# Performance work log

Hardware: AMD Instinct MI355X
Metric: run time of the kernel (lower is better)

The kernel has to match this reference:

```python
import jax, jax.numpy as jnp
import numpy as np

B, T, C = 2, 4096, 768
H = 12
D = C // H  # head_dim = 64
SCALE = np.sqrt(D).astype(np.float32)


def setup_inputs() -> dict:
    key = jax.random.key(0)
    ks = jax.random.split(key, 5)
    s = 0.02
    return {
        "x": jax.random.normal(ks[0], (B, T, C), dtype=jnp.float32),
        "Wqkv": jax.random.normal(ks[1], (C, 3 * C), dtype=jnp.float32) * s,
        "bqkv": jnp.zeros((3 * C,), dtype=jnp.float32),
        "Wout": jax.random.normal(ks[2], (C, C), dtype=jnp.float32) * s,
        "bout": jnp.zeros((C,), dtype=jnp.float32),
    }


def reference(x, Wqkv, bqkv, Wout, bout):
    Bx, Tx, Cx = x.shape
    qkv = x @ Wqkv + bqkv                                   # [B,T,3C]
    qkv = qkv.reshape(Bx, Tx, 3, H, D)
    q, k, v = [jnp.moveaxis(qkv[:, :, i], 2, 1) for i in range(3)]  # each [B,H,T,D]
    attn = jnp.einsum("bhqd,bhkd->bhqk", q, k) / SCALE      # [B,H,T,T]
    causal = jnp.tril(jnp.ones((Tx, Tx), dtype=bool))
    attn = jnp.where(causal, attn, jnp.float32(-jnp.inf))
    attn = jax.nn.softmax(attn, axis=-1)
    out = jnp.einsum("bhqk,bhkd->bhqd", attn, v)            # [B,H,T,D]
    out = jnp.moveaxis(out, 1, 2).reshape(Bx, Tx, Cx)       # [B,T,C]
    return out @ Wout + bout
```

## Files before the change

### kernel.cpp

```cpp
#include <hip/hip_runtime.h>
#include <hip/hip_bf16.h>

#define T_DIM 4096
#define H_N 12
#define D_H 64
#define C_DIM 768
#define B_N 2

typedef short bf16x8 __attribute__((ext_vector_type(8)));
typedef float f32x4 __attribute__((ext_vector_type(4)));
typedef float f32x16 __attribute__((ext_vector_type(16)));

__device__ __forceinline__ short f2bf(float f) {
    union { float f; unsigned u; } x; x.f = f;
    unsigned r = x.u + 0x7fffu + ((x.u >> 16) & 1u);
    return (short)(r >> 16);
}
__device__ __forceinline__ unsigned pk2bf(float a, float b) {
    union { float f; unsigned u; } x, y; x.f = a; y.f = b;
    unsigned ua = x.u + 0x7fffu + ((x.u >> 16) & 1u);
    unsigned ub = y.u + 0x7fffu + ((y.u >> 16) & 1u);
    return (ua >> 16) | (ub & 0xffff0000u);
}
__device__ __forceinline__ unsigned pktrunc(float lo, float hi) {
    union { float f; unsigned u; } a, b; a.f = lo; b.f = hi;
    return __builtin_amdgcn_perm(b.u, a.u, 0x07060302u);
}
__device__ __forceinline__ float bf2f(short s) {
    union { unsigned u; float f; } x; x.u = ((unsigned)(unsigned short)s) << 16;
    return x.f;
}

__device__ __forceinline__ void async_copy16(const void* g, void* l) {
    __builtin_amdgcn_global_load_lds(
        (const __attribute__((address_space(1))) unsigned*)g,
        (__attribute__((address_space(3))) unsigned*)l, 16, 0, 0);
}

#define Q_SCALE 0.18033688011112042f

#define CHUNK 1152
#define UNITS_PB 74
#define SLOTS_PB 74

__device__ __forceinline__ void wtrans_body(
    const float* __restrict__ W, short* __restrict__ Wt, int K, int N,
    int bx, int by, int tid)
{
    const int wave = tid >> 6, lane = tid & 63;
    const int n = bx * 256 + wave * 64 + lane;
    const int k0 = by * 128;
    for (int k = k0; k < k0 + 128; k += 8) {
        unsigned pk[4];
#pragma unroll
        for (int j = 0; j < 4; ++j)
            pk[j] = pk2bf(W[(size_t)(k + 2 * j) * N + n],
                          W[(size_t)(k + 2 * j + 1) * N + n]);
        *(uint4*)(Wt + (size_t)n * K + k) = *(uint4*)pk;
    }
}

__global__ __launch_bounds__(256) void prep_kernel(
    const float* __restrict__ x, short* __restrict__ xb,
    const float* __restrict__ Wqkv, short* __restrict__ Wqkvb,
    const float* __restrict__ Wout, short* __restrict__ Woutb)
{
    const int bid = blockIdx.x;
    const int tid = threadIdx.x;
    if (bid < 3072) {
        size_t i = ((size_t)bid * 256 + tid) * 8;
        float4 a = *(const float4*)(x + i);
        float4 b = *(const float4*)(x + i + 4);
        unsigned pk[4];
        pk[0] = pk2bf(a.x, a.y); pk[1] = pk2bf(a.z, a.w);
        pk[2] = pk2bf(b.x, b.y); pk[3] = pk2bf(b.z, b.w);
        *(uint4*)(xb + i) = *(uint4*)pk;
    } else if (bid < 3126) {
        int u = bid - 3072;
        wtrans_body(Wqkv, Wqkvb, 768, 2304, u % 9, u / 9, tid);
    } else {
        int u = bid - 3126;
        wtrans_body(Wout, Woutb, 768, 768, u % 3, u / 3, tid);
    }
}

__global__ __launch_bounds__(256) void qkv_kernel(
    const short* __restrict__ xb, const short* __restrict__ Wb,
    const float* __restrict__ bias,
    short* __restrict__ Qo, short* __restrict__ Ko, short* __restrict__ Vto)
{
    __shared__ short As[128 * 32];
    __shared__ short Bs[128 * 32];
    __shared__ short Vs[64][136];

    const int tid  = threadIdx.x;
    const int wave = tid >> 6, lane = tid & 63;
    const int quad = lane >> 4, l16 = lane & 15;
    const int wm = wave >> 1, wn = wave & 1;
    const int lin = blockIdx.x;
    const int xcd = lin & 7, idx = lin >> 3;
    const int m0 = (xcd * 8 + (idx & 7)) * 128;
    const int n0 = (idx >> 3) * 128;
    const int lrow = lane >> 2, lcc = lane & 3;

    f32x4 acc[4][4];
#pragma unroll
    for (int i = 0; i < 4; ++i)
#pragma unroll
        for (int j = 0; j < 4; ++j) acc[i][j] = (f32x4){0.f, 0.f, 0.f, 0.f};

    for (int k0 = 0; k0 < 768; k0 += 32) {
        __syncthreads();
#pragma unroll
        for (int i = 0; i < 2; ++i) {
            const int sbase = wave * 128 + i * 64;
            const int row = wave * 32 + i * 16 + lrow;
            async_copy16(xb + (size_t)(m0 + row) * 768 + k0 + lcc * 8, &As[sbase * 8]);
            async_copy16(Wb + (size_t)(n0 + row) * 768 + k0 + lcc * 8, &Bs[sbase * 8]);
        }
        asm volatile("s_waitcnt vmcnt(0)" ::: "memory");
        __syncthreads();

        bf16x8 af[4], bfr[4];
#pragma unroll
        for (int t = 0; t < 4; ++t)
            af[t] = *(const bf16x8*)&As[(wm * 64 + t * 16 + l16) * 32 + quad * 8];
#pragma unroll
        for (int t = 0; t < 4; ++t)
            bfr[t] = *(const bf16x8*)&Bs[(wn * 64 + t * 16 + l16) * 32 + quad * 8];
#pragma unroll
        for (int mt = 0; mt < 4; ++mt)
#pragma unroll
            for (int nt = 0; nt < 4; ++nt)
                acc[mt][nt] = __builtin_amdgcn_mfma_f32_16x16x32_bf16(
                    af[mt], bfr[nt], acc[mt][nt], 0, 0, 0);
    }

    if (n0 < 1536) {
#pragma unroll
        for (int nt = 0; nt < 4; ++nt) {
            int n = n0 + wn * 64 + nt * 16 + l16;
            float bv = bias[n];
            int which = n >= 768;
            int cw = n - which * 768;
            int h = cw >> 6, d = cw & 63;
            float scale = which ? 1.0f : Q_SCALE;
            short* dst = which ? Ko : Qo;
#pragma unroll
            for (int mt = 0; mt < 4; ++mt) {
#pragma unroll
                for (int reg = 0; reg < 4; ++reg) {
                    int m = m0 + wm * 64 + mt * 16 + quad * 4 + reg;
                    int b = m >> 12, t = m & 4095;
                    dst[(size_t)((b * H_N + h) * T_DIM + t) * D_H + d] =
                        f2bf((acc[mt][nt][reg] + bv) * scale);
                }
            }
        }
    } else {
        const int b = m0 >> 12, t0 = m0 & 4095;
        for (int p = 0; p < 2; ++p) {
            if (wn == p) {
#pragma unroll
                for (int nt = 0; nt < 4; ++nt) {
                    int n = n0 + wn * 64 + nt * 16 + l16;
                    float bv = bias[n];
#pragma unroll
                    for (int mt = 0; mt < 4; ++mt)
#pragma unroll
                        for (int reg = 0; reg < 4; ++reg)
                            Vs[nt * 16 + l16][wm * 64 + mt * 16 + quad * 4 + reg] =
                                f2bf(acc[mt][nt][reg] + bv);
                }
            }
            __syncthreads();
            int hh = ((n0 - 1536) >> 6) + p;
#pragma unroll
            for (int cc = tid; cc < 512; cc += 256) {
                int d = cc >> 3, part = cc & 7;
                bf16x8 v0 = *(const bf16x8*)&Vs[d][part * 16];
                bf16x8 v1 = *(const bf16x8*)&Vs[d][part * 16 + 8];
                size_t dst = ((size_t)(b * H_N + hh) * D_H + d) * T_DIM + t0 + part * 16;
                *(bf16x8*)(Vto + dst) = v0;
                *(bf16x8*)(Vto + dst + 8) = v1;
            }
            __syncthreads();
        }
    }
}

template<bool EDGE>
__device__ __forceinline__ void attn_tile(
    const short* __restrict__ Kb, const short* __restrict__ Vb,
    const bf16x8 (&qf)[4], const bf16x8& ones,
    f32x16& oacc0, f32x16& oacc1, f32x16& lacc,
    int kv0, int row0, int l32, int hi, int qrow)
{
#pragma unroll
    for (int sub = 0; sub < 2; ++sub) {
        if (EDGE && (kv0 + sub * 32 > row0 + 31)) continue;

        f32x16 sacc;
#pragma unroll
        for (int r = 0; r < 16; ++r) sacc[r] = 0.f;
        const int R = sub * 32 + l32;
        __builtin_amdgcn_s_setprio(1);
#pragma unroll
        for (int dk = 0; dk < 4; ++dk) {
            bf16x8 kf = *(const bf16x8*)
                &Kb[(R * 8 + ((dk * 2 + hi) ^ (R & 7))) * 8];
            sacc = __builtin_amdgcn_mfma_f32_32x32x16_bf16(kf, qf[dk], sacc, 0, 0, 0);
        }
        __builtin_amdgcn_s_setprio(0);

        if (EDGE && (kv0 + sub * 32 + 31 > row0)) {
#pragma unroll
            for (int r = 0; r < 16; ++r) {
                int kvg = kv0 + sub * 32 + (r & 3) + 8 * (r >> 2) + 4 * hi;
                if (kvg > qrow) sacc[r] = -1e30f;
            }
        }

        unsigned w[8];
#pragma unroll
        for (int r2 = 0; r2 < 8; ++r2)
            w[r2] = pktrunc(exp2f(sacc[2 * r2]), exp2f(sacc[2 * r2 + 1]));

        asm volatile("v_permlane32_swap_b32 %0, %1" : "+v"(w[0]), "+v"(w[2]));
        asm volatile("v_permlane32_swap_b32 %0, %1" : "+v"(w[1]), "+v"(w[3]));
        asm volatile("v_permlane32_swap_b32 %0, %1" : "+v"(w[4]), "+v"(w[6]));
        asm volatile("v_permlane32_swap_b32 %0, %1" : "+v"(w[5]), "+v"(w[7]));
        union { unsigned u[4]; bf16x8 v; } af0, af1;
        af0.u[0] = w[0]; af0.u[1] = w[1]; af0.u[2] = w[2]; af0.u[3] = w[3];
        af1.u[0] = w[4]; af1.u[1] = w[5]; af1.u[2] = w[6]; af1.u[3] = w[7];

        __builtin_amdgcn_s_setprio(1);
        lacc = __builtin_amdgcn_mfma_f32_32x32x16_bf16(af0.v, ones, lacc, 0, 0, 0);
        lacc = __builtin_amdgcn_mfma_f32_32x32x16_bf16(af1.v, ones, lacc, 0, 0, 0);

#pragma unroll
        for (int kh = 0; kh < 2; ++kh) {
            bf16x8 pa = kh ? af1.v : af0.v;
#pragma unroll
            for (int dt = 0; dt < 2; ++dt) {
                int Rv = dt * 32 + l32;
                bf16x8 vf = *(const bf16x8*)
                    &Vb[(Rv * 8 + ((sub * 4 + kh * 2 + hi) ^ (Rv & 7))) * 8];
                f32x16& oa = dt ? oacc1 : oacc0;
                oa = __builtin_amdgcn_mfma_f32_32x32x16_bf16(pa, vf, oa, 0, 0, 0);
            }
        }
        __builtin_amdgcn_s_setprio(0);
    }
}

__global__ __launch_bounds__(256, 4) void attn_partial_kernel(
    const short* __restrict__ Q, const short* __restrict__ K,
    const short* __restrict__ Vt, short* __restrict__ Opart,
    float* __restrict__ Lbuf)
{
    __shared__ short KsT[2][4096];
    __shared__ short VsT[2][4096];

    const int tid  = threadIdx.x;
    const int wave = tid >> 6, lane = tid & 63;
    const int l32 = lane & 31, hi = lane >> 5;
    const int lin = blockIdx.x;
    const int xcd = lin & 7, idx = lin >> 3;
    const int bh = xcd + ((idx / UNITS_PB) << 3);
    const int rr = idx % UNITS_PB;

    int qj, ci;
    if (rr < 9)       { qj = 9 + rr; ci = 0; }
    else if (rr < 27) { int u = rr - 9;  qj = 18 + (u >> 1); ci = u & 1; }
    else if (rr < 42) { int u = rr - 27; qj = 27 + u / 3; ci = u % 3; }
    else if (rr < 54) { int t = rr - 42; int m = 8 - t / 3; int idxm = t % 3;
                        qj = m + 9 * idxm; ci = idxm; }
    else              { int t = rr - 54; int m = 4 - (t >> 2); int idxm = t & 3;
                        qj = m + 9 * idxm; ci = idxm; }

    const int q0 = qj * 128;
    const int kvStart = ci * CHUNK;
    const int kvEnd = min(kvStart + CHUNK, q0 + 128);
    const int ntiles = (kvEnd - kvStart) >> 6;
    const int off = (qj < 9)  ? qj
                  : (qj < 18) ? 9 + (qj - 9) * 2
                  : (qj < 27) ? 27 + (qj - 18) * 3
                              : 54 + (qj - 27) * 4;
    const int s = bh * SLOTS_PB + off + ci;
    const size_t base = (size_t)bh * T_DIM * D_H;
    const int row0 = q0 + wave * 32;
    const int qrow = row0 + l32;

    const int nfull = min(ntiles, max(0, (row0 - kvStart + 1) >> 6));

    bf16x8 qf[4];
#pragma unroll
    for (int dk = 0; dk < 4; ++dk)
        qf[dk] = *(const bf16x8*)(
            Q + base + (size_t)(row0 + l32) * 64 + dk * 16 + hi * 8);

    bf16x8 ones;
#pragma unroll
    for (int j = 0; j < 8; ++j) ones[j] = (short)0x3F80;

    f32x16 oacc0, oacc1, lacc;
#pragma unroll
    for (int r = 0; r < 16; ++r) { oacc0[r] = 0.f; oacc1[r] = 0.f; lacc[r] = 0.f; }

    const int srow = (wave * 128 + lane) >> 3;
    const int scol0 = (lane & 7) ^ (srow & 7);
    const int srow1 = (wave * 128 + 64 + lane) >> 3;
    const int scol1 = (lane & 7) ^ (srow1 & 7);

    {
        const int kv0 = kvStart;
        async_copy16(K + base + (size_t)(kv0 + srow) * 64 + scol0 * 8,
                     &KsT[0][(wave * 128) * 8]);
        async_copy16(Vt + base + (size_t)srow * T_DIM + kv0 + scol0 * 8,
                     &VsT[0][(wave * 128) * 8]);
        async_copy16(K + base + (size_t)(kv0 + srow1) * 64 + scol1 * 8,
                     &KsT[0][(wave * 128 + 64) * 8]);
        async_copy16(Vt + base + (size_t)srow1 * T_DIM + kv0 + scol1 * 8,
                     &VsT[0][(wave * 128 + 64) * 8]);
    }

    int buf = 0;
    for (int it = 0; it < ntiles; ++it) {
        const int kv0 = kvStart + it * 64;

        asm volatile("s_waitcnt vmcnt(0)" ::: "memory");
        asm volatile("s_barrier" ::: "memory");

        if (it + 1 < ntiles) {
            const int kn = kv0 + 64;
            async_copy16(K + base + (size_t)(kn + srow) * 64 + scol0 * 8,
                         &KsT[buf ^ 1][(wave * 128) * 8]);
            async_copy16(Vt + base + (size_t)srow * T_DIM + kn + scol0 * 8,
                         &VsT[buf ^ 1][(wave * 128) * 8]);
            async_copy16(K + base + (size_t)(kn + srow1) * 64 + scol1 * 8,
                         &KsT[buf ^ 1][(wave * 128 + 64) * 8]);
            async_copy16(Vt + base + (size_t)srow1 * T_DIM + kn + scol1 * 8,
                         &VsT[buf ^ 1][(wave * 128 + 64) * 8]);
        }

        if (it < nfull) {
            attn_tile<false>(&KsT[buf][0], &VsT[buf][0], qf, ones,
                             oacc0, oacc1, lacc, kv0, row0, l32, hi, qrow);
        } else if (kv0 <= row0 + 31) {
            attn_tile<true>(&KsT[buf][0], &VsT[buf][0], qf, ones,
                            oacc0, oacc1, lacc, kv0, row0, l32, hi, qrow);
        }
        buf ^= 1;
    }

    short* op = Opart + (size_t)s * 8192;
#pragma unroll
    for (int r = 0; r < 16; ++r) {
        int qr = wave * 32 + (r & 3) + 8 * (r >> 2) + 4 * hi;
        op[qr * 64 + l32]      = f2bf(oacc0[r]);
        op[qr * 64 + 32 + l32] = f2bf(oacc1[r]);
    }
    if (l32 == 0) {
#pragma unroll
        for (int r = 0; r < 16; ++r)
            Lbuf[s * 128 + wave * 32 + (r & 3) + 8 * (r >> 2) + 4 * hi] = lacc[r];
    }
}

__global__ __launch_bounds__(256) void combine_kernel(
    const short* __restrict__ Opart, const float* __restrict__ Lbuf,
    short* __restrict__ O)
{
    const int tid = threadIdx.x;
    const int qi = blockIdx.x, bh = blockIdx.y;
    const int b = bh / H_N, h = bh - b * H_N;
    const int r = tid >> 2, cg = (tid & 3) * 16;
    const int qj = qi >> 1;
    const int riu = (qi & 1) * 64 + r;
    const int off = (qj < 9)  ? qj
                  : (qj < 18) ? 9 + (qj - 9) * 2
                  : (qj < 27) ? 27 + (qj - 18) * 3
                              : 54 + (qj - 27) * 4;
    const int nc = qj / 9 + 1;
    const int s0 = bh * SLOTS_PB + off;

    float l = 0.f;
    float res[16];
#pragma unroll
    for (int j = 0; j < 16; ++j) res[j] = 0.f;

    for (int ci = 0; ci < nc; ++ci) {
        const int su = s0 + ci;
        l += Lbuf[su * 128 + riu];
        const short* p = Opart + (size_t)su * 8192 + riu * 64 + cg;
        bf16x8 a0 = *(const bf16x8*)p;
        bf16x8 a1 = *(const bf16x8*)(p + 8);
#pragma unroll
        for (int j = 0; j < 8; ++j) { res[j] += bf2f(a0[j]); res[8 + j] += bf2f(a1[j]); }
    }

    float inv = 1.0f / l;
    unsigned pk[8];
#pragma unroll
    for (int j = 0; j < 8; ++j) pk[j] = pk2bf(res[2 * j] * inv, res[2 * j + 1] * inv);
    size_t o = ((size_t)b * T_DIM + qi * 64 + r) * C_DIM + h * 64 + cg;
    *(uint4*)(O + o)     = *(uint4*)&pk[0];
    *(uint4*)(O + o + 8) = *(uint4*)&pk[4];
}

__global__ __launch_bounds__(256) void out_kernel(
    const short* __restrict__ A, const short* __restrict__ Wb,
    const float* __restrict__ bias, float* __restrict__ out)
{
    __shared__ short As[64 * 32];
    __shared__ short Bs[128 * 32];

    const int tid  = threadIdx.x;
    const int wave = tid >> 6, lane = tid & 63;
    const int quad = lane >> 4, l16 = lane & 15;
    const int wm = wave >> 1, wn = wave & 1;
    const int lin = blockIdx.x;
    const int xcd = lin & 7, idx = lin >> 3;
    const int m0 = (xcd * 16 + (idx & 15)) * 64;
    const int n0 = (idx >> 4) * 128;
    const int lrow = lane >> 2, lcc = lane & 3;
    const int aRow = wave * 16 + lrow;

    f32x4 acc[2][4];
#pragma unroll
    for (int i = 0; i < 2; ++i)
#pragma unroll
        for (int j = 0; j < 4; ++j) acc[i][j] = (f32x4){0.f, 0.f, 0.f, 0.f};

    for (int k0 = 0; k0 < 768; k0 += 32) {
        __syncthreads();
        async_copy16(A + (size_t)(m0 + aRow) * 768 + k0 + lcc * 8, &As[wave * 512]);
#pragma unroll
        for (int i = 0; i < 2; ++i) {
            const int sbase = wave * 128 + i * 64;
            const int row = wave * 32 + i * 16 + lrow;
            async_copy16(Wb + (size_t)(n0 + row) * 768 + k0 + lcc * 8, &Bs[sbase * 8]);
        }
        asm volatile("s_waitcnt vmcnt(0)" ::: "memory");
        __syncthreads();

        bf16x8 af[2], bfr[4];
#pragma unroll
        for (int t = 0; t < 2; ++t)
            af[t] = *(const bf16x8*)&As[(wm * 32 + t * 16 + l16) * 32 + quad * 8];
#pragma unroll
        for (int t = 0; t < 4; ++t)
            bfr[t] = *(const bf16x8*)&Bs[(wn * 64 + t * 16 + l16) * 32 + quad * 8];
#pragma unroll
        for (int mt = 0; mt < 2; ++mt)
#pragma unroll
            for (int nt = 0; nt < 4; ++nt)
                acc[mt][nt] = __builtin_amdgcn_mfma_f32_16x16x32_bf16(
                    af[mt], bfr[nt], acc[mt][nt], 0, 0, 0);
    }

#pragma unroll
    for (int nt = 0; nt < 4; ++nt) {
        int n = n0 + wn * 64 + nt * 16 + l16;
        float bv = bias[n];
#pragma unroll
        for (int mt = 0; mt < 2; ++mt) {
#pragma unroll
            for (int reg = 0; reg < 4; ++reg) {
                int m = m0 + wm * 32 + mt * 16 + quad * 4 + reg;
                out[(size_t)m * 768 + n] = acc[mt][nt][reg] + bv;
            }
        }
    }
}

extern "C" void kernel_launch(void* const* d_in, const int* in_sizes, int n_in,
                              void* d_out, int out_size, void* d_ws, size_t ws_size,
                              hipStream_t stream) {
    const float* x    = (const float*)d_in[0];
    const float* Wqkv = (const float*)d_in[1];
    const float* bqkv = (const float*)d_in[2];
    const float* Wout = (const float*)d_in[3];
    const float* bout = (const float*)d_in[4];
    float* out = (float*)d_out;

    const size_t per = (size_t)B_N * H_N * T_DIM * D_H;
    short* Q      = (short*)d_ws;
    short* K      = Q + per;
    short* Vt     = K + per;
    short* Woutb  = Vt + per;
    short* xb     = Woutb + (size_t)768 * 768;
    short* Wqkvb  = xb + per;
    short* Opart  = xb;
    float* Lbuf   = (float*)(Opart + (size_t)24 * SLOTS_PB * 8192);
    short* O      = Q;

    prep_kernel<<<dim3(3144), 256, 0, stream>>>(x, xb, Wqkv, Wqkvb, Wout, Woutb);
    qkv_kernel<<<dim3(1152), 256, 0, stream>>>(xb, Wqkvb, bqkv, Q, K, Vt);
    attn_partial_kernel<<<dim3(UNITS_PB * 24), 256, 0, stream>>>(Q, K, Vt, Opart, Lbuf);
    combine_kernel<<<dim3(64, 24), 256, 0, stream>>>(Opart, Lbuf, O);
    out_kernel<<<dim3(768), 256, 0, stream>>>(O, Woutb, bout, out);
}
```

Measured before the change: 282.6 us.

## Fuse split-KV combine into output projection GEMM A-tile load

Removes the separate combine kernel. The output projection kernel now sums the partial attention outputs and normalises them by the summed softmax denominators while building its A tile in shared memory. This drops one launch and the write and re-read of the intermediate O buffer. In exchange, each of the 6 N-tile blocks sharing an M tile repeats the partial-sum reduction, and the A-tile loads become synchronous instead of async copies.

```diff
diff --git a/kernel.cpp b/kernel.cpp
--- a/kernel.cpp
+++ b/kernel.cpp
@@ -368,53 +368,14 @@
     }
 }
 
-__global__ __launch_bounds__(256) void combine_kernel(
+__global__ __launch_bounds__(256) void out_kernel(
     const short* __restrict__ Opart, const float* __restrict__ Lbuf,
-    short* __restrict__ O)
-{
-    const int tid = threadIdx.x;
-    const int qi = blockIdx.x, bh = blockIdx.y;
-    const int b = bh / H_N, h = bh - b * H_N;
-    const int r = tid >> 2, cg = (tid & 3) * 16;
-    const int qj = qi >> 1;
-    const int riu = (qi & 1) * 64 + r;
-    const int off = (qj < 9)  ? qj
-                  : (qj < 18) ? 9 + (qj - 9) * 2
-                  : (qj < 27) ? 27 + (qj - 18) * 3
-                              : 54 + (qj - 27) * 4;
-    const int nc = qj / 9 + 1;
-    const int s0 = bh * SLOTS_PB + off;
-
-    float l = 0.f;
-    float res[16];
-#pragma unroll
-    for (int j = 0; j < 16; ++j) res[j] = 0.f;
-
-    for (int ci = 0; ci < nc; ++ci) {
-        const int su = s0 + ci;
-        l += Lbuf[su * 128 + riu];
-        const short* p = Opart + (size_t)su * 8192 + riu * 64 + cg;
-        bf16x8 a0 = *(const bf16x8*)p;
-        bf16x8 a1 = *(const bf16x8*)(p + 8);
-#pragma unroll
-        for (int j = 0; j < 8; ++j) { res[j] += bf2f(a0[j]); res[8 + j] += bf2f(a1[j]); }
-    }
-
-    float inv = 1.0f / l;
-    unsigned pk[8];
-#pragma unroll
-    for (int j = 0; j < 8; ++j) pk[j] = pk2bf(res[2 * j] * inv, res[2 * j + 1] * inv);
-    size_t o = ((size_t)b * T_DIM + qi * 64 + r) * C_DIM + h * 64 + cg;
-    *(uint4*)(O + o)     = *(uint4*)&pk[0];
-    *(uint4*)(O + o + 8) = *(uint4*)&pk[4];
-}
-
-__global__ __launch_bounds__(256) void out_kernel(
-    const short* __restrict__ A, const short* __restrict__ Wb,
-    const float* __restrict__ bias, float* __restrict__ out)
+    const short* __restrict__ Wb, const float* __restrict__ bias,
+    float* __restrict__ out)
 {
     __shared__ short As[64 * 32];
     __shared__ short Bs[128 * 32];
+    __shared__ float invl[12 * 64];
 
     const int tid  = threadIdx.x;
     const int wave = tid >> 6, lane = tid & 63;
@@ -425,7 +386,26 @@
     const int m0 = (xcd * 16 + (idx & 15)) * 64;
     const int n0 = (idx >> 4) * 128;
     const int lrow = lane >> 2, lcc = lane & 3;
-    const int aRow = wave * 16 + lrow;
+
+    const int b    = m0 >> 12;
+    const int t0   = m0 & 4095;
+    const int qj   = t0 >> 7;
+    const int half = (t0 >> 6) & 1;
+    const int off = (qj < 9)  ? qj
+                  : (qj < 18) ? 9 + (qj - 9) * 2
+                  : (qj < 27) ? 27 + (qj - 18) * 3
+                              : 54 + (qj - 27) * 4;
+    const int nc = qj / 9 + 1;
+
+    for (int ii = tid; ii < 768; ii += 256) {
+        int h = ii >> 6, r = ii & 63;
+        float l = 0.f;
+        for (int ci = 0; ci < nc; ++ci)
+            l += Lbuf[((b * H_N + h) * SLOTS_PB + off + ci) * 128 + half * 64 + r];
+        invl[ii] = 1.0f / l;
+    }
+
+    const int ar = tid >> 2, adp = tid & 3;
 
     f32x4 acc[2][4];
 #pragma unroll
@@ -435,13 +415,33 @@
 
     for (int k0 = 0; k0 < 768; k0 += 32) {
         __syncthreads();
-        async_copy16(A + (size_t)(m0 + aRow) * 768 + k0 + lcc * 8, &As[wave * 512]);
+
 #pragma unroll
         for (int i = 0; i < 2; ++i) {
             const int sbase = wave * 128 + i * 64;
             const int row = wave * 32 + i * 16 + lrow;
             async_copy16(Wb + (size_t)(n0 + row) * 768 + k0 + lcc * 8, &Bs[sbase * 8]);
         }
+
+        const int h = k0 >> 6, d0 = k0 & 63;
+        const short* ap = Opart
+            + ((size_t)(b * H_N + h) * SLOTS_PB + off) * 8192
+            + (half * 64 + ar) * 64 + d0 + adp * 8;
+        float sum[8];
+#pragma unroll
+        for (int j = 0; j < 8; ++j) sum[j] = 0.f;
+        for (int ci = 0; ci < nc; ++ci) {
+            bf16x8 a = *(const bf16x8*)(ap + ci * 8192);
+#pragma unroll
+            for (int j = 0; j < 8; ++j) sum[j] += bf2f(a[j]);
+        }
+        float sc = invl[h * 64 + ar];
+        unsigned pk[4];
+#pragma unroll
+        for (int j = 0; j < 4; ++j)
+            pk[j] = pk2bf(sum[2 * j] * sc, sum[2 * j + 1] * sc);
+        *(uint4*)&As[ar * 32 + adp * 8] = *(uint4*)pk;
+
         asm volatile("s_waitcnt vmcnt(0)" ::: "memory");
         __syncthreads();
 
@@ -494,11 +494,9 @@
     short* Wqkvb  = xb + per;
     short* Opart  = xb;
     float* Lbuf   = (float*)(Opart + (size_t)24 * SLOTS_PB * 8192);
-    short* O      = Q;
 
     prep_kernel<<<dim3(3144), 256, 0, stream>>>(x, xb, Wqkv, Wqkvb, Wout, Woutb);
     qkv_kernel<<<dim3(1152), 256, 0, stream>>>(xb, Wqkvb, bqkv, Q, K, Vt);
     attn_partial_kernel<<<dim3(UNITS_PB * 24), 256, 0, stream>>>(Q, K, Vt, Opart, Lbuf);
-    combine_kernel<<<dim3(64, 24), 256, 0, stream>>>(Opart, Lbuf, O);
-    out_kernel<<<dim3(768), 256, 0, stream>>>(O, Woutb, bout, out);
-}
+    out_kernel<<<dim3(768), 256, 0, stream>>>(Opart, Lbuf, Woutb, bout, out);
+}
```

After: 298.4 us. +5.6%, slower.
